# Kernel tuning notes

Measured on AMD Instinct MI355X. Metric: run time of the kernel, lower is better.

Reference implementation:

```python
import jax, jax.numpy as jnp
import numpy as np

# Model/config constants
N = 2048          # total nodes in batch
G = 32            # number of graphs
NPG = 64          # nodes per graph (N = G * NPG)
E = 16384         # total edges (E//G per graph, unique within graph)
HIDDEN = 256
N_HEADS = 8
HEAD_DIM = HIDDEN // N_HEADS
EDGE_FEAT = 16
SCALE = HEAD_DIM ** -0.5


def setup_inputs() -> dict:
    key = jax.random.key(0)
    ks = jax.random.split(key, 16)
    nodes = jax.random.normal(ks[0], (N, HIDDEN), dtype=jnp.float32)
    edges = jax.random.normal(ks[1], (E, EDGE_FEAT), dtype=jnp.float32)
    n_node = jnp.full((G,), NPG, dtype=jnp.int32)
    # Unique (sender, receiver) pairs within each graph block
    epg = E // G
    gkeys = jax.random.split(ks[2], G)
    perm = jax.vmap(lambda k: jax.random.permutation(k, NPG * NPG)[:epg])(gkeys)  # [G, epg]
    so = perm // NPG
    ro = perm % NPG
    base = (jnp.arange(G, dtype=jnp.int32) * NPG)[:, None]
    senders = (base + so).reshape(-1).astype(jnp.int32)
    receivers = (base + ro).reshape(-1).astype(jnp.int32)
    init = 0.02
    Wq = jax.random.normal(ks[3], (HIDDEN, HIDDEN), jnp.float32) * init
    Wk = jax.random.normal(ks[4], (HIDDEN, HIDDEN), jnp.float32) * init
    Wv = jax.random.normal(ks[5], (HIDDEN, HIDDEN), jnp.float32) * init
    Wo = jax.random.normal(ks[6], (HIDDEN, HIDDEN), jnp.float32) * init
    We = jax.random.normal(ks[7], (EDGE_FEAT, N_HEADS), jnp.float32) * init
    bq = jnp.zeros((HIDDEN,), jnp.float32)
    bk = jnp.zeros((HIDDEN,), jnp.float32)
    bv = jnp.zeros((HIDDEN,), jnp.float32)
    bo = jnp.zeros((HIDDEN,), jnp.float32)
    be = jnp.zeros((N_HEADS,), jnp.float32)
    return {"nodes": nodes, "edges": edges, "n_node": n_node,
            "senders": senders, "receivers": receivers,
            "Wq": Wq, "bq": bq, "Wk": Wk, "bk": bk, "Wv": Wv, "bv": bv,
            "Wo": Wo, "bo": bo, "We": We, "be": be}


def reference(nodes, edges, n_node, senders, receivers,
              Wq, bq, Wk, bk, Wv, bv, Wo, bo, We, be):
    n_nodes = nodes.shape[0]
    n_graphs = n_node.shape[0]
    q = (nodes @ Wq + bq).reshape(n_nodes, N_HEADS, HEAD_DIM)
    k = (nodes @ Wk + bk).reshape(n_nodes, N_HEADS, HEAD_DIM)
    v = (nodes @ Wv + bv).reshape(n_nodes, N_HEADS, HEAD_DIM)
    scores = jnp.einsum('ihd,jhd->ijh', q, k) * SCALE  # [N, N, H]
    graph_idx = jnp.repeat(jnp.arange(n_graphs), n_node, total_repeat_length=n_nodes)
    same_graph = graph_idx[:, None] == graph_idx[None, :]
    scores = scores + jnp.where(same_graph[:, :, None], 0.0, -1e9)
    # Edge bias scattered into [N, N, H] at (receiver, sender)
    edge_bias = edges @ We + be  # [E, H]
    edge_bias_matrix = jnp.zeros((n_nodes, n_nodes, N_HEADS), dtype=scores.dtype)
    edge_bias_matrix = edge_bias_matrix.at[receivers, senders].set(edge_bias)
    scores = scores + edge_bias_matrix
    attn = jax.nn.softmax(scores, axis=1)  # softmax over key axis j
    out = jnp.einsum('ijh,jhd->ihd', attn, v).reshape(n_nodes, HIDDEN)
    return out @ Wo + bo
```

## Files before the change

kernel.cpp:

```cpp
#include <hip/hip_runtime.h>

#define N_NODES 2048
#define N_GRAPHS 32
#define NPG 64
#define N_EDGES 16384
#define EPG 512
#define HIDDEN 256
#define NHEADS 8
#define HEADDIM 32
#define EDGEFEAT 16
#define ATT_SCALE 0.17677669529663687f

typedef unsigned short u16;
typedef __attribute__((ext_vector_type(8))) short bf16x8;
typedef __attribute__((ext_vector_type(4))) float f32x4;

__device__ __forceinline__ u16 f2b(float f) {
    unsigned x = __float_as_uint(f);
    return (u16)((x + 0x7fffu + ((x >> 16) & 1u)) >> 16);
}
__device__ __forceinline__ float b2f(u16 u) {
    return __uint_as_float(((unsigned)u) << 16);
}
__device__ __forceinline__ unsigned pack2(float a, float b) {
    return (unsigned)f2b(a) | ((unsigned)f2b(b) << 16);
}

__global__ __launch_bounds__(256)
void setup_pre(const float* __restrict__ Wq, const float* __restrict__ Wk,
               const float* __restrict__ Wv, const float* __restrict__ Wo,
               const float* __restrict__ edges, const float* __restrict__ We,
               const float* __restrict__ be,
               const int* __restrict__ senders, const int* __restrict__ receivers,
               u16* __restrict__ WT,
               uint2* __restrict__ ebp)
{
    const int b = blockIdx.x, tid = threadIdx.x;
    __shared__ float sf[64 * 65];

    if (b < 64) {
        const int m = b >> 4, tile = b & 15;
        const int k0 = (tile >> 2) * 64, n0 = (tile & 3) * 64;
        const float* src = (m == 0) ? Wq : (m == 1) ? Wk : (m == 2) ? Wv : Wo;
        u16* dst = WT + m * 65536;
        #pragma unroll
        for (int i = 0; i < 4; ++i) {
            const int idx = i * 256 + tid, kr = idx >> 4, c4 = idx & 15;
            float4 x = *(const float4*)(src + (size_t)(k0 + kr) * HIDDEN + n0 + c4 * 4);
            sf[kr * 65 + c4 * 4 + 0] = x.x;
            sf[kr * 65 + c4 * 4 + 1] = x.y;
            sf[kr * 65 + c4 * 4 + 2] = x.z;
            sf[kr * 65 + c4 * 4 + 3] = x.w;
        }
        __syncthreads();
        #pragma unroll
        for (int i = 0; i < 4; ++i) {
            const int idx = i * 256 + tid, nr = idx >> 4, c4 = idx & 15;
            uint2 w;
            w.x = pack2(sf[(c4 * 4 + 0) * 65 + nr], sf[(c4 * 4 + 1) * 65 + nr]);
            w.y = pack2(sf[(c4 * 4 + 2) * 65 + nr], sf[(c4 * 4 + 3) * 65 + nr]);
            *(uint2*)&dst[(size_t)(n0 + nr) * HIDDEN + k0 + c4 * 4] = w;
        }
    } else {
        float* sWe = sf;
        float* sbe = sf + 128;
        if (tid < 128) sWe[tid] = We[tid];
        if (tid < 8)  sbe[tid] = be[tid];
        __syncthreads();
        const int e = (b - 64) * 256 + tid;
        const float* ep = edges + (size_t)e * EDGEFEAT;
        float4 f0 = *(const float4*)(ep + 0);
        float4 f1 = *(const float4*)(ep + 4);
        float4 f2 = *(const float4*)(ep + 8);
        float4 f3 = *(const float4*)(ep + 12);
        const float ef[16] = {f0.x, f0.y, f0.z, f0.w, f1.x, f1.y, f1.z, f1.w,
                              f2.x, f2.y, f2.z, f2.w, f3.x, f3.y, f3.z, f3.w};
        const unsigned idx =
            (unsigned)((receivers[e] & (NPG - 1)) * 65 + (senders[e] & (NPG - 1)));
        #pragma unroll
        for (int h = 0; h < NHEADS; ++h) {
            float bias = sbe[h];
            #pragma unroll
            for (int f = 0; f < EDGEFEAT; ++f) bias += ef[f] * sWe[f * 8 + h];
            ebp[(size_t)h * N_EDGES + e] = make_uint2(__float_as_uint(bias), idx);
        }
    }
}

__global__ __launch_bounds__(256)
void attn_fused(const float* __restrict__ nodes,
                const u16* __restrict__ WT,
                const float* __restrict__ bq, const float* __restrict__ bk,
                const float* __restrict__ bv,
                const uint2* __restrict__ ebp,
                u16* __restrict__ attnb)
{
    const int g = blockIdx.x, h = blockIdx.y;
    const int tid = threadIdx.x;
    const int lane = tid & 63, wvi = tid >> 6;
    const int l16 = lane & 15, quad = lane >> 4;

    __shared__ __align__(16) unsigned char smem[43776];
    short* qhi = (short*)smem;
    short* qlo = qhi + 2560;
    short* khi = qlo + 2560;
    short* klo = khi + 2560;
    short* vsT = klo + 2560;
    float* sc  = (float*)(smem + 25088);
    float* red = sc + 64 * 65;

    const uint2 e0 = ebp[(size_t)h * N_EDGES + g * EPG + tid];
    const uint2 e1 = ebp[(size_t)h * N_EDGES + g * EPG + 256 + tid];
    float biasv[6];
    #pragma unroll
    for (int nt = 0; nt < 6; ++nt) {
        const int tns = nt >> 1;
        const float* bp = (tns == 0) ? bq : (tns == 1) ? bk : bv;
        biasv[nt] = bp[h * HEADDIM + (nt & 1) * 16 + l16];
    }

    f32x4 acc[6];
    #pragma unroll
    for (int nt = 0; nt < 6; ++nt) acc[nt] = (f32x4){0.f, 0.f, 0.f, 0.f};
    const float* Arow = nodes + (size_t)(g * NPG + wvi * 16 + l16) * HIDDEN + quad * 8;
    #pragma unroll
    for (int k0 = 0; k0 < HIDDEN; k0 += 32) {
        float4 xa = *(const float4*)(Arow + k0);
        float4 xb = *(const float4*)(Arow + k0 + 4);
        uint4 ua;
        ua.x = pack2(xa.x, xa.y);
        ua.y = pack2(xa.z, xa.w);
        ua.z = pack2(xb.x, xb.y);
        ua.w = pack2(xb.z, xb.w);
        bf16x8 af = *(bf16x8*)&ua;
        #pragma unroll
        for (int nt = 0; nt < 6; ++nt) {
            const u16* bp = WT + (nt >> 1) * 65536
                          + (size_t)(h * HEADDIM + (nt & 1) * 16 + l16) * HIDDEN
                          + k0 + quad * 8;
            acc[nt] = __builtin_amdgcn_mfma_f32_16x16x32_bf16(
                af, *(const bf16x8*)bp, acc[nt], 0, 0, 0);
        }
    }

    #pragma unroll
    for (int nt = 0; nt < 6; ++nt) {
        const int tns = nt >> 1;
        const int col = (nt & 1) * 16 + l16;
        #pragma unroll
        for (int r = 0; r < 4; ++r) {
            const int row = wvi * 16 + quad * 4 + r;
            const float val = acc[nt][r] + biasv[nt];
            if (tns == 2) {
                vsT[col * 72 + row] = (short)f2b(val);
            } else {
                const u16 hi = f2b(val);
                const u16 lo = f2b(val - b2f(hi));
                if (tns == 0) { qhi[row * 40 + col] = (short)hi; qlo[row * 40 + col] = (short)lo; }
                else          { khi[row * 40 + col] = (short)hi; klo[row * 40 + col] = (short)lo; }
            }
        }
    }
    __syncthreads();

    {
        bf16x8 qh = *(const bf16x8*)&qhi[(wvi * 16 + l16) * 40 + quad * 8];
        bf16x8 ql = *(const bf16x8*)&qlo[(wvi * 16 + l16) * 40 + quad * 8];
        #pragma unroll
        for (int nt = 0; nt < 4; ++nt) {
            bf16x8 kh = *(const bf16x8*)&khi[(nt * 16 + l16) * 40 + quad * 8];
            bf16x8 kl = *(const bf16x8*)&klo[(nt * 16 + l16) * 40 + quad * 8];
            f32x4 s = (f32x4){0.f, 0.f, 0.f, 0.f};
            s = __builtin_amdgcn_mfma_f32_16x16x32_bf16(qh, kh, s, 0, 0, 0);
            s = __builtin_amdgcn_mfma_f32_16x16x32_bf16(qh, kl, s, 0, 0, 0);
            s = __builtin_amdgcn_mfma_f32_16x16x32_bf16(ql, kh, s, 0, 0, 0);
            #pragma unroll
            for (int r = 0; r < 4; ++r)
                sc[(wvi * 16 + quad * 4 + r) * 65 + nt * 16 + l16] = s[r] * ATT_SCALE;
        }
    }
    __syncthreads();

    sc[e0.y] += __uint_as_float(e0.x);
    sc[e1.y] += __uint_as_float(e1.x);
    __syncthreads();

    {
        const int i  = tid & 63;
        const int cg = tid >> 6;
        float* red_m = red;
        float* red_s = red + 4 * 64;
        float m = -1e30f;
        #pragma unroll
        for (int jj = 0; jj < 16; ++jj) m = fmaxf(m, sc[i * 65 + cg * 16 + jj]);
        red_m[cg * 64 + i] = m;
        __syncthreads();
        m = fmaxf(fmaxf(red_m[0 * 64 + i], red_m[1 * 64 + i]),
                  fmaxf(red_m[2 * 64 + i], red_m[3 * 64 + i]));
        float s = 0.f;
        #pragma unroll
        for (int jj = 0; jj < 16; ++jj) {
            const int j = cg * 16 + jj;
            float e = __expf(sc[i * 65 + j] - m);
            sc[i * 65 + j] = e;
            s += e;
        }
        red_s[cg * 64 + i] = s;
        __syncthreads();
        const float inv = 1.f / (red_s[0 * 64 + i] + red_s[1 * 64 + i] +
                                 red_s[2 * 64 + i] + red_s[3 * 64 + i]);
        #pragma unroll
        for (int jj = 0; jj < 16; ++jj) sc[i * 65 + cg * 16 + jj] *= inv;
    }
    __syncthreads();

    {
        f32x4 oacc[2];
        oacc[0] = (f32x4){0.f, 0.f, 0.f, 0.f};
        oacc[1] = (f32x4){0.f, 0.f, 0.f, 0.f};
        #pragma unroll
        for (int k0 = 0; k0 < NPG; k0 += 32) {
            float p[8];
            #pragma unroll
            for (int jj = 0; jj < 8; ++jj)
                p[jj] = sc[(wvi * 16 + l16) * 65 + k0 + quad * 8 + jj];
            uint4 uh, ul;
            u16 h0 = f2b(p[0]), h1 = f2b(p[1]), h2 = f2b(p[2]), h3 = f2b(p[3]);
            u16 h4 = f2b(p[4]), h5 = f2b(p[5]), h6 = f2b(p[6]), h7 = f2b(p[7]);
            uh.x = (unsigned)h0 | ((unsigned)h1 << 16);
            uh.y = (unsigned)h2 | ((unsigned)h3 << 16);
            uh.z = (unsigned)h4 | ((unsigned)h5 << 16);
            uh.w = (unsigned)h6 | ((unsigned)h7 << 16);
            ul.x = pack2(p[0] - b2f(h0), p[1] - b2f(h1));
            ul.y = pack2(p[2] - b2f(h2), p[3] - b2f(h3));
            ul.z = pack2(p[4] - b2f(h4), p[5] - b2f(h5));
            ul.w = pack2(p[6] - b2f(h6), p[7] - b2f(h7));
            bf16x8 ph = *(bf16x8*)&uh;
            bf16x8 pl = *(bf16x8*)&ul;
            #pragma unroll
            for (int nt = 0; nt < 2; ++nt) {
                bf16x8 vf = *(const bf16x8*)&vsT[(nt * 16 + l16) * 72 + k0 + quad * 8];
                oacc[nt] = __builtin_amdgcn_mfma_f32_16x16x32_bf16(ph, vf, oacc[nt], 0, 0, 0);
                oacc[nt] = __builtin_amdgcn_mfma_f32_16x16x32_bf16(pl, vf, oacc[nt], 0, 0, 0);
            }
        }
        #pragma unroll
        for (int nt = 0; nt < 2; ++nt) {
            const int d = nt * 16 + l16;
            #pragma unroll
            for (int r = 0; r < 4; ++r) {
                const int row = wvi * 16 + quad * 4 + r;
                attnb[(size_t)(g * NPG + row) * HIDDEN + h * HEADDIM + d] =
                    f2b(oacc[nt][r]);
            }
        }
    }
}

__global__ __launch_bounds__(256)
void outproj(const u16* __restrict__ A,
             const u16* __restrict__ WoT,
             const float* __restrict__ bo,
             float* __restrict__ C)
{
    const int n0 = blockIdx.x * 32, m0 = blockIdx.y * 64;
    const int tid = threadIdx.x;
    const int lane = tid & 63, wvi = tid >> 6;
    const int l16 = lane & 15, quad = lane >> 4;

    f32x4 acc[2];
    acc[0] = (f32x4){0.f, 0.f, 0.f, 0.f};
    acc[1] = (f32x4){0.f, 0.f, 0.f, 0.f};
    const u16* Ar = A + (size_t)(m0 + wvi * 16 + l16) * HIDDEN + quad * 8;
    #pragma unroll
    for (int k0 = 0; k0 < HIDDEN; k0 += 32) {
        bf16x8 af = *(const bf16x8*)(Ar + k0);
        #pragma unroll
        for (int nt = 0; nt < 2; ++nt) {
            const u16* bp = WoT + (size_t)(n0 + nt * 16 + l16) * HIDDEN + k0 + quad * 8;
            acc[nt] = __builtin_amdgcn_mfma_f32_16x16x32_bf16(
                af, *(const bf16x8*)bp, acc[nt], 0, 0, 0);
        }
    }
    #pragma unroll
    for (int nt = 0; nt < 2; ++nt) {
        const int col = n0 + nt * 16 + l16;
        const float bias = bo[col];
        #pragma unroll
        for (int r = 0; r < 4; ++r)
            C[(size_t)(m0 + wvi * 16 + quad * 4 + r) * HIDDEN + col] = acc[nt][r] + bias;
    }
}

extern "C" void kernel_launch(void* const* d_in, const int* in_sizes, int n_in,
                              void* d_out, int out_size, void* d_ws, size_t ws_size,
                              hipStream_t stream)
{
    const float* nodes     = (const float*)d_in[0];
    const float* edges     = (const float*)d_in[1];
    const int*   senders   = (const int*)d_in[3];
    const int*   receivers = (const int*)d_in[4];
    const float* Wq = (const float*)d_in[5];
    const float* bq = (const float*)d_in[6];
    const float* Wk = (const float*)d_in[7];
    const float* bk = (const float*)d_in[8];
    const float* Wv = (const float*)d_in[9];
    const float* bv = (const float*)d_in[10];
    const float* Wo = (const float*)d_in[11];
    const float* bo = (const float*)d_in[12];
    const float* We = (const float*)d_in[13];
    const float* be = (const float*)d_in[14];
    float* out = (float*)d_out;

    u16*   WT     = (u16*)d_ws;
    uint2* ebp    = (uint2*)((char*)d_ws + 524288);
    u16*   attnb  = (u16*)((char*)d_ws + 1572864);

    setup_pre<<<dim3(128), dim3(256), 0, stream>>>(
        Wq, Wk, Wv, Wo, edges, We, be, senders, receivers, WT, ebp);
    attn_fused<<<dim3(N_GRAPHS, NHEADS), dim3(256), 0, stream>>>(
        nodes, WT, bq, bk, bv, ebp, attnb);
    outproj<<<dim3(HIDDEN / 32, N_NODES / 64), dim3(256), 0, stream>>>(
        attnb, WT + 3 * 65536, bo, out);
}
```

Before: 99.91 us.

## Fuse edge-bias computation into attention kernel and double its waves per block

```diff
diff --git a/kernel.cpp b/kernel.cpp
--- a/kernel.cpp
+++ b/kernel.cpp
@@ -27,80 +27,54 @@
 }
 
 __global__ __launch_bounds__(256)
-void setup_pre(const float* __restrict__ Wq, const float* __restrict__ Wk,
-               const float* __restrict__ Wv, const float* __restrict__ Wo,
-               const float* __restrict__ edges, const float* __restrict__ We,
-               const float* __restrict__ be,
-               const int* __restrict__ senders, const int* __restrict__ receivers,
-               u16* __restrict__ WT,
-               uint2* __restrict__ ebp)
+void setup_wt(const float* __restrict__ Wq, const float* __restrict__ Wk,
+              const float* __restrict__ Wv, const float* __restrict__ Wo,
+              u16* __restrict__ WT)
 {
     const int b = blockIdx.x, tid = threadIdx.x;
     __shared__ float sf[64 * 65];
 
-    if (b < 64) {
-        const int m = b >> 4, tile = b & 15;
-        const int k0 = (tile >> 2) * 64, n0 = (tile & 3) * 64;
-        const float* src = (m == 0) ? Wq : (m == 1) ? Wk : (m == 2) ? Wv : Wo;
-        u16* dst = WT + m * 65536;
-        #pragma unroll
-        for (int i = 0; i < 4; ++i) {
-            const int idx = i * 256 + tid, kr = idx >> 4, c4 = idx & 15;
-            float4 x = *(const float4*)(src + (size_t)(k0 + kr) * HIDDEN + n0 + c4 * 4);
-            sf[kr * 65 + c4 * 4 + 0] = x.x;
-            sf[kr * 65 + c4 * 4 + 1] = x.y;
-            sf[kr * 65 + c4 * 4 + 2] = x.z;
-            sf[kr * 65 + c4 * 4 + 3] = x.w;
-        }
-        __syncthreads();
-        #pragma unroll
-        for (int i = 0; i < 4; ++i) {
-            const int idx = i * 256 + tid, nr = idx >> 4, c4 = idx & 15;
-            uint2 w;
-            w.x = pack2(sf[(c4 * 4 + 0) * 65 + nr], sf[(c4 * 4 + 1) * 65 + nr]);
-            w.y = pack2(sf[(c4 * 4 + 2) * 65 + nr], sf[(c4 * 4 + 3) * 65 + nr]);
-            *(uint2*)&dst[(size_t)(n0 + nr) * HIDDEN + k0 + c4 * 4] = w;
-        }
-    } else {
-        float* sWe = sf;
-        float* sbe = sf + 128;
-        if (tid < 128) sWe[tid] = We[tid];
-        if (tid < 8)  sbe[tid] = be[tid];
-        __syncthreads();
-        const int e = (b - 64) * 256 + tid;
-        const float* ep = edges + (size_t)e * EDGEFEAT;
-        float4 f0 = *(const float4*)(ep + 0);
-        float4 f1 = *(const float4*)(ep + 4);
-        float4 f2 = *(const float4*)(ep + 8);
-        float4 f3 = *(const float4*)(ep + 12);
-        const float ef[16] = {f0.x, f0.y, f0.z, f0.w, f1.x, f1.y, f1.z, f1.w,
-                              f2.x, f2.y, f2.z, f2.w, f3.x, f3.y, f3.z, f3.w};
-        const unsigned idx =
-            (unsigned)((receivers[e] & (NPG - 1)) * 65 + (senders[e] & (NPG - 1)));
-        #pragma unroll
-        for (int h = 0; h < NHEADS; ++h) {
-            float bias = sbe[h];
-            #pragma unroll
-            for (int f = 0; f < EDGEFEAT; ++f) bias += ef[f] * sWe[f * 8 + h];
-            ebp[(size_t)h * N_EDGES + e] = make_uint2(__float_as_uint(bias), idx);
-        }
-    }
-}
-
-__global__ __launch_bounds__(256)
+    const int m = b >> 4, tile = b & 15;
+    const int k0 = (tile >> 2) * 64, n0 = (tile & 3) * 64;
+    const float* src = (m == 0) ? Wq : (m == 1) ? Wk : (m == 2) ? Wv : Wo;
+    u16* dst = WT + m * 65536;
+    #pragma unroll
+    for (int i = 0; i < 4; ++i) {
+        const int idx = i * 256 + tid, kr = idx >> 4, c4 = idx & 15;
+        float4 x = *(const float4*)(src + (size_t)(k0 + kr) * HIDDEN + n0 + c4 * 4);
+        sf[kr * 65 + c4 * 4 + 0] = x.x;
+        sf[kr * 65 + c4 * 4 + 1] = x.y;
+        sf[kr * 65 + c4 * 4 + 2] = x.z;
+        sf[kr * 65 + c4 * 4 + 3] = x.w;
+    }
+    __syncthreads();
+    #pragma unroll
+    for (int i = 0; i < 4; ++i) {
+        const int idx = i * 256 + tid, nr = idx >> 4, c4 = idx & 15;
+        uint2 w2;
+        w2.x = pack2(sf[(c4 * 4 + 0) * 65 + nr], sf[(c4 * 4 + 1) * 65 + nr]);
+        w2.y = pack2(sf[(c4 * 4 + 2) * 65 + nr], sf[(c4 * 4 + 3) * 65 + nr]);
+        *(uint2*)&dst[(size_t)(n0 + nr) * HIDDEN + k0 + c4 * 4] = w2;
+    }
+}
+
+__global__ __launch_bounds__(512)
 void attn_fused(const float* __restrict__ nodes,
                 const u16* __restrict__ WT,
                 const float* __restrict__ bq, const float* __restrict__ bk,
                 const float* __restrict__ bv,
-                const uint2* __restrict__ ebp,
+                const float* __restrict__ edges, const float* __restrict__ We,
+                const float* __restrict__ be,
+                const int* __restrict__ senders, const int* __restrict__ receivers,
                 u16* __restrict__ attnb)
 {
     const int g = blockIdx.x, h = blockIdx.y;
     const int tid = threadIdx.x;
-    const int lane = tid & 63, wvi = tid >> 6;
+    const int lane = tid & 63, w = tid >> 6;
     const int l16 = lane & 15, quad = lane >> 4;
-
-    __shared__ __align__(16) unsigned char smem[43776];
+    const int stripe = w & 3, grp = w >> 2;
+
+    __shared__ __align__(16) unsigned char smem[45824];
     short* qhi = (short*)smem;
     short* qlo = qhi + 2560;
     short* khi = qlo + 2560;
@@ -108,21 +82,34 @@
     short* vsT = klo + 2560;
     float* sc  = (float*)(smem + 25088);
     float* red = sc + 64 * 65;
-
-    const uint2 e0 = ebp[(size_t)h * N_EDGES + g * EPG + tid];
-    const uint2 e1 = ebp[(size_t)h * N_EDGES + g * EPG + 256 + tid];
-    float biasv[6];
-    #pragma unroll
-    for (int nt = 0; nt < 6; ++nt) {
+    __shared__ float we_h[EDGEFEAT];
+    __shared__ float sbe;
+
+    if (tid < EDGEFEAT) we_h[tid] = We[tid * NHEADS + h];
+    if (tid == 0) sbe = be[h];
+
+    const int e = g * EPG + tid;
+    const float* ep = edges + (size_t)e * EDGEFEAT;
+    const float4 ef0 = *(const float4*)(ep + 0);
+    const float4 ef1 = *(const float4*)(ep + 4);
+    const float4 ef2 = *(const float4*)(ep + 8);
+    const float4 ef3 = *(const float4*)(ep + 12);
+    const int s_l = senders[e] & (NPG - 1);
+    const int r_l = receivers[e] & (NPG - 1);
+
+    float biasv[3];
+    #pragma unroll
+    for (int j = 0; j < 3; ++j) {
+        const int nt = grp * 3 + j;
         const int tns = nt >> 1;
         const float* bp = (tns == 0) ? bq : (tns == 1) ? bk : bv;
-        biasv[nt] = bp[h * HEADDIM + (nt & 1) * 16 + l16];
-    }
-
-    f32x4 acc[6];
-    #pragma unroll
-    for (int nt = 0; nt < 6; ++nt) acc[nt] = (f32x4){0.f, 0.f, 0.f, 0.f};
-    const float* Arow = nodes + (size_t)(g * NPG + wvi * 16 + l16) * HIDDEN + quad * 8;
+        biasv[j] = bp[h * HEADDIM + (nt & 1) * 16 + l16];
+    }
+
+    f32x4 acc[3];
+    #pragma unroll
+    for (int j = 0; j < 3; ++j) acc[j] = (f32x4){0.f, 0.f, 0.f, 0.f};
+    const float* Arow = nodes + (size_t)(g * NPG + stripe * 16 + l16) * HIDDEN + quad * 8;
     #pragma unroll
     for (int k0 = 0; k0 < HIDDEN; k0 += 32) {
         float4 xa = *(const float4*)(Arow + k0);
@@ -134,23 +121,25 @@
         ua.w = pack2(xb.z, xb.w);
         bf16x8 af = *(bf16x8*)&ua;
         #pragma unroll
-        for (int nt = 0; nt < 6; ++nt) {
+        for (int j = 0; j < 3; ++j) {
+            const int nt = grp * 3 + j;
             const u16* bp = WT + (nt >> 1) * 65536
                           + (size_t)(h * HEADDIM + (nt & 1) * 16 + l16) * HIDDEN
                           + k0 + quad * 8;
-            acc[nt] = __builtin_amdgcn_mfma_f32_16x16x32_bf16(
-                af, *(const bf16x8*)bp, acc[nt], 0, 0, 0);
-        }
-    }
-
-    #pragma unroll
-    for (int nt = 0; nt < 6; ++nt) {
+            acc[j] = __builtin_amdgcn_mfma_f32_16x16x32_bf16(
+                af, *(const bf16x8*)bp, acc[j], 0, 0, 0);
+        }
+    }
+
+    #pragma unroll
+    for (int j = 0; j < 3; ++j) {
+        const int nt = grp * 3 + j;
         const int tns = nt >> 1;
         const int col = (nt & 1) * 16 + l16;
         #pragma unroll
         for (int r = 0; r < 4; ++r) {
-            const int row = wvi * 16 + quad * 4 + r;
-            const float val = acc[nt][r] + biasv[nt];
+            const int row = stripe * 16 + quad * 4 + r;
+            const float val = acc[j][r] + biasv[j];
             if (tns == 2) {
                 vsT[col * 72 + row] = (short)f2b(val);
             } else {
@@ -164,10 +153,11 @@
     __syncthreads();
 
     {
-        bf16x8 qh = *(const bf16x8*)&qhi[(wvi * 16 + l16) * 40 + quad * 8];
-        bf16x8 ql = *(const bf16x8*)&qlo[(wvi * 16 + l16) * 40 + quad * 8];
-        #pragma unroll
-        for (int nt = 0; nt < 4; ++nt) {
+        bf16x8 qh = *(const bf16x8*)&qhi[(stripe * 16 + l16) * 40 + quad * 8];
+        bf16x8 ql = *(const bf16x8*)&qlo[(stripe * 16 + l16) * 40 + quad * 8];
+        #pragma unroll
+        for (int t = 0; t < 2; ++t) {
+            const int nt = grp * 2 + t;
             bf16x8 kh = *(const bf16x8*)&khi[(nt * 16 + l16) * 40 + quad * 8];
             bf16x8 kl = *(const bf16x8*)&klo[(nt * 16 + l16) * 40 + quad * 8];
             f32x4 s = (f32x4){0.f, 0.f, 0.f, 0.f};
@@ -176,54 +166,61 @@
             s = __builtin_amdgcn_mfma_f32_16x16x32_bf16(ql, kh, s, 0, 0, 0);
             #pragma unroll
             for (int r = 0; r < 4; ++r)
-                sc[(wvi * 16 + quad * 4 + r) * 65 + nt * 16 + l16] = s[r] * ATT_SCALE;
-        }
-    }
-    __syncthreads();
-
-    sc[e0.y] += __uint_as_float(e0.x);
-    sc[e1.y] += __uint_as_float(e1.x);
+                sc[(stripe * 16 + quad * 4 + r) * 65 + nt * 16 + l16] = s[r] * ATT_SCALE;
+        }
+    }
+    __syncthreads();
+
+    {
+        const float b = sbe
+            + ef0.x * we_h[0]  + ef0.y * we_h[1]  + ef0.z * we_h[2]  + ef0.w * we_h[3]
+            + ef1.x * we_h[4]  + ef1.y * we_h[5]  + ef1.z * we_h[6]  + ef1.w * we_h[7]
+            + ef2.x * we_h[8]  + ef2.y * we_h[9]  + ef2.z * we_h[10] + ef2.w * we_h[11]
+            + ef3.x * we_h[12] + ef3.y * we_h[13] + ef3.z * we_h[14] + ef3.w * we_h[15];
+        sc[r_l * 65 + s_l] += b;
+    }
     __syncthreads();
 
     {
         const int i  = tid & 63;
         const int cg = tid >> 6;
         float* red_m = red;
-        float* red_s = red + 4 * 64;
+        float* red_s = red + 8 * 64;
         float m = -1e30f;
         #pragma unroll
-        for (int jj = 0; jj < 16; ++jj) m = fmaxf(m, sc[i * 65 + cg * 16 + jj]);
+        for (int jj = 0; jj < 8; ++jj) m = fmaxf(m, sc[i * 65 + cg * 8 + jj]);
         red_m[cg * 64 + i] = m;
         __syncthreads();
-        m = fmaxf(fmaxf(red_m[0 * 64 + i], red_m[1 * 64 + i]),
-                  fmaxf(red_m[2 * 64 + i], red_m[3 * 64 + i]));
+        #pragma unroll
+        for (int c = 0; c < 8; ++c) m = fmaxf(m, red_m[c * 64 + i]);
         float s = 0.f;
         #pragma unroll
-        for (int jj = 0; jj < 16; ++jj) {
-            const int j = cg * 16 + jj;
-            float e = __expf(sc[i * 65 + j] - m);
-            sc[i * 65 + j] = e;
-            s += e;
+        for (int jj = 0; jj < 8; ++jj) {
+            const int j = cg * 8 + jj;
+            float ev = __expf(sc[i * 65 + j] - m);
+            sc[i * 65 + j] = ev;
+            s += ev;
         }
         red_s[cg * 64 + i] = s;
         __syncthreads();
-        const float inv = 1.f / (red_s[0 * 64 + i] + red_s[1 * 64 + i] +
-                                 red_s[2 * 64 + i] + red_s[3 * 64 + i]);
-        #pragma unroll
-        for (int jj = 0; jj < 16; ++jj) sc[i * 65 + cg * 16 + jj] *= inv;
+        float den = red_s[0 * 64 + i];
+        #pragma unroll
+        for (int c = 1; c < 8; ++c) den += red_s[c * 64 + i];
+        const float inv = 1.f / den;
+        #pragma unroll
+        for (int jj = 0; jj < 8; ++jj) sc[i * 65 + cg * 8 + jj] *= inv;
     }
     __syncthreads();
 
     {
-        f32x4 oacc[2];
-        oacc[0] = (f32x4){0.f, 0.f, 0.f, 0.f};
-        oacc[1] = (f32x4){0.f, 0.f, 0.f, 0.f};
+        const int nt = grp;
+        f32x4 oacc = (f32x4){0.f, 0.f, 0.f, 0.f};
         #pragma unroll
         for (int k0 = 0; k0 < NPG; k0 += 32) {
             float p[8];
             #pragma unroll
             for (int jj = 0; jj < 8; ++jj)
-                p[jj] = sc[(wvi * 16 + l16) * 65 + k0 + quad * 8 + jj];
+                p[jj] = sc[(stripe * 16 + l16) * 65 + k0 + quad * 8 + jj];
             uint4 uh, ul;
             u16 h0 = f2b(p[0]), h1 = f2b(p[1]), h2 = f2b(p[2]), h3 = f2b(p[3]);
             u16 h4 = f2b(p[4]), h5 = f2b(p[5]), h6 = f2b(p[6]), h7 = f2b(p[7]);
@@ -237,22 +234,15 @@
             ul.w = pack2(p[6] - b2f(h6), p[7] - b2f(h7));
             bf16x8 ph = *(bf16x8*)&uh;
             bf16x8 pl = *(bf16x8*)&ul;
-            #pragma unroll
-            for (int nt = 0; nt < 2; ++nt) {
-                bf16x8 vf = *(const bf16x8*)&vsT[(nt * 16 + l16) * 72 + k0 + quad * 8];
-                oacc[nt] = __builtin_amdgcn_mfma_f32_16x16x32_bf16(ph, vf, oacc[nt], 0, 0, 0);
-                oacc[nt] = __builtin_amdgcn_mfma_f32_16x16x32_bf16(pl, vf, oacc[nt], 0, 0, 0);
-            }
-        }
-        #pragma unroll
-        for (int nt = 0; nt < 2; ++nt) {
-            const int d = nt * 16 + l16;
-            #pragma unroll
-            for (int r = 0; r < 4; ++r) {
-                const int row = wvi * 16 + quad * 4 + r;
-                attnb[(size_t)(g * NPG + row) * HIDDEN + h * HEADDIM + d] =
-                    f2b(oacc[nt][r]);
-            }
+            bf16x8 vf = *(const bf16x8*)&vsT[(nt * 16 + l16) * 72 + k0 + quad * 8];
+            oacc = __builtin_amdgcn_mfma_f32_16x16x32_bf16(ph, vf, oacc, 0, 0, 0);
+            oacc = __builtin_amdgcn_mfma_f32_16x16x32_bf16(pl, vf, oacc, 0, 0, 0);
+        }
+        const int d = nt * 16 + l16;
+        #pragma unroll
+        for (int r = 0; r < 4; ++r) {
+            const int row = stripe * 16 + quad * 4 + r;
+            attnb[(size_t)(g * NPG + row) * HIDDEN + h * HEADDIM + d] = f2b(oacc[r]);
         }
     }
 }
@@ -263,33 +253,26 @@
              const float* __restrict__ bo,
              float* __restrict__ C)
 {
-    const int n0 = blockIdx.x * 32, m0 = blockIdx.y * 64;
+    const int bid = blockIdx.x;
+    const int n0 = (bid & 7) * 32, m0 = (bid >> 3) * 32;
     const int tid = threadIdx.x;
-    const int lane = tid & 63, wvi = tid >> 6;
+    const int lane = tid & 63, w = tid >> 6;
     const int l16 = lane & 15, quad = lane >> 4;
-
-    f32x4 acc[2];
-    acc[0] = (f32x4){0.f, 0.f, 0.f, 0.f};
-    acc[1] = (f32x4){0.f, 0.f, 0.f, 0.f};
-    const u16* Ar = A + (size_t)(m0 + wvi * 16 + l16) * HIDDEN + quad * 8;
+    const int mst = w & 1, nt = w >> 1;
+
+    f32x4 acc = (f32x4){0.f, 0.f, 0.f, 0.f};
+    const u16* Ar = A   + (size_t)(m0 + mst * 16 + l16) * HIDDEN + quad * 8;
+    const u16* Br = WoT + (size_t)(n0 + nt  * 16 + l16) * HIDDEN + quad * 8;
     #pragma unroll
     for (int k0 = 0; k0 < HIDDEN; k0 += 32) {
-        bf16x8 af = *(const bf16x8*)(Ar + k0);
-        #pragma unroll
-        for (int nt = 0; nt < 2; ++nt) {
-            const u16* bp = WoT + (size_t)(n0 + nt * 16 + l16) * HIDDEN + k0 + quad * 8;
-            acc[nt] = __builtin_amdgcn_mfma_f32_16x16x32_bf16(
-                af, *(const bf16x8*)bp, acc[nt], 0, 0, 0);
-        }
-    }
-    #pragma unroll
-    for (int nt = 0; nt < 2; ++nt) {
-        const int col = n0 + nt * 16 + l16;
-        const float bias = bo[col];
-        #pragma unroll
-        for (int r = 0; r < 4; ++r)
-            C[(size_t)(m0 + wvi * 16 + quad * 4 + r) * HIDDEN + col] = acc[nt][r] + bias;
-    }
+        acc = __builtin_amdgcn_mfma_f32_16x16x32_bf16(
+            *(const bf16x8*)(Ar + k0), *(const bf16x8*)(Br + k0), acc, 0, 0, 0);
+    }
+    const int col = n0 + nt * 16 + l16;
+    const float bias = bo[col];
+    #pragma unroll
+    for (int r = 0; r < 4; ++r)
+        C[(size_t)(m0 + mst * 16 + quad * 4 + r) * HIDDEN + col] = acc[r] + bias;
 }
 
 extern "C" void kernel_launch(void* const* d_in, const int* in_sizes, int n_in,
@@ -312,14 +295,12 @@
     const float* be = (const float*)d_in[14];
     float* out = (float*)d_out;
 
-    u16*   WT     = (u16*)d_ws;
-    uint2* ebp    = (uint2*)((char*)d_ws + 524288);
-    u16*   attnb  = (u16*)((char*)d_ws + 1572864);
-
-    setup_pre<<<dim3(128), dim3(256), 0, stream>>>(
-        Wq, Wk, Wv, Wo, edges, We, be, senders, receivers, WT, ebp);
-    attn_fused<<<dim3(N_GRAPHS, NHEADS), dim3(256), 0, stream>>>(
-        nodes, WT, bq, bk, bv, ebp, attnb);
-    outproj<<<dim3(HIDDEN / 32, N_NODES / 64), dim3(256), 0, stream>>>(
+    u16* WT    = (u16*)d_ws;
+    u16* attnb = (u16*)((char*)d_ws + 524288);
+
+    setup_wt<<<dim3(64), dim3(256), 0, stream>>>(Wq, Wk, Wv, Wo, WT);
+    attn_fused<<<dim3(N_GRAPHS, NHEADS), dim3(512), 0, stream>>>(
+        nodes, WT, bq, bk, bv, edges, We, be, senders, receivers, attnb);
+    outproj<<<dim3(512), dim3(256), 0, stream>>>(
         attnb, WT + 3 * 65536, bo, out);
 }
```

New measurement: 102.5 us. 2.6% more time.
